# Kernel tuning notes

Hardware: AMD Instinct MI355X
Metric: run time of the kernel (lower is better)

Reference implementation:

```python
import jax, jax.numpy as jnp
import numpy as np

DIM, HEADS, DHEAD = 256, 8, 64
INNER = HEADS * DHEAD
EPS = 1e-5


def _ln(x, g, b):
    m = x.mean(-1, keepdims=True)
    v = ((x - m) ** 2).mean(-1, keepdims=True)
    return (x - m) / jnp.sqrt(v + EPS) * g + b


def setup_inputs() -> dict:
    key = jax.random.key(0)
    ks = jax.random.split(key, 24)
    b, n, Q, K = 1, 6, 900, 1408
    d = DIM
    s = lambda fan_in: 1.0 / np.sqrt(fan_in)
    inp = {
        "k_g": jax.random.normal(ks[0], (b, n, K, d), jnp.float32),
        "q_g": jax.random.normal(ks[1], (b, n, Q, d), jnp.float32),
        "k_a": jax.random.normal(ks[2], (b, n, K, d), jnp.float32),
        "q_a": jax.random.normal(ks[3], (b, Q, d), jnp.float32),
        "v": jax.random.normal(ks[4], (b, n, K, d), jnp.float32),
        "mask": jax.random.randint(ks[5], (b, n, K), 0, 2).astype(bool),
        # projections (stored as (in, out))
        "W_qg": jax.random.uniform(ks[6], (d, INNER), jnp.float32, -s(d), s(d)),
        "b_qg": jnp.zeros((INNER,), jnp.float32),
        "W_kg": jax.random.uniform(ks[7], (d, INNER), jnp.float32, -s(d), s(d)),
        "b_kg": jnp.zeros((INNER,), jnp.float32),
        "W_qa": jax.random.uniform(ks[8], (d, INNER), jnp.float32, -s(d), s(d)),
        "b_qa": jnp.zeros((INNER,), jnp.float32),
        "W_ka": jax.random.uniform(ks[9], (d, INNER), jnp.float32, -s(d), s(d)),
        "b_ka": jnp.zeros((INNER,), jnp.float32),
        "W_v": jax.random.uniform(ks[10], (d, INNER), jnp.float32, -s(d), s(d)),
        "b_v": jnp.zeros((INNER,), jnp.float32),
        "W_o": jax.random.uniform(ks[11], (INNER, d), jnp.float32, -s(INNER), s(INNER)),
        "b_o": jnp.zeros((d,), jnp.float32),
        "ln1_g": jnp.ones((d,), jnp.float32),
        "ln1_b": jnp.zeros((d,), jnp.float32),
        "W_m1": jax.random.uniform(ks[12], (d, 2 * d), jnp.float32, -s(d), s(d)),
        "b_m1": jnp.zeros((2 * d,), jnp.float32),
        "W_m2": jax.random.uniform(ks[13], (2 * d, d), jnp.float32, -s(2 * d), s(2 * d)),
        "b_m2": jnp.zeros((d,), jnp.float32),
        "ln2_g": jnp.ones((d,), jnp.float32),
        "ln2_b": jnp.zeros((d,), jnp.float32),
        "scale_g": jnp.full((HEADS,), DHEAD ** -0.5, jnp.float32),
        "scale_a": jnp.full((HEADS,), DHEAD ** -0.5, jnp.float32),
    }
    return inp


def reference(k_g, q_g, k_a, q_a, v, mask,
              W_qg, b_qg, W_kg, b_kg, W_qa, b_qa, W_ka, b_ka, W_v, b_v,
              W_o, b_o, ln1_g, ln1_b, W_m1, b_m1, W_m2, b_m2, ln2_g, ln2_b,
              scale_g, scale_a):
    b, n, Q, _ = q_g.shape
    K = k_g.shape[2]
    h, dh = HEADS, DHEAD
    skip = q_a

    def split(x):  # (..., h*dh) -> (b, h, ..., dh)
        return jnp.moveaxis(x.reshape(x.shape[:-1] + (h, dh)), -2, 1)

    kg = split(k_g @ W_kg + b_kg)          # (b, h, n, K, dh)
    qg = split(q_g @ W_qg + b_qg)          # (b, h, n, Q, dh)
    ka = split(k_a @ W_ka + b_ka)          # (b, h, n, K, dh)
    qa = split(q_a @ W_qa + b_qa)          # (b, h, Q, dh)
    vv = split(v @ W_v + b_v)              # (b, h, n, K, dh)

    dot_g = jnp.einsum('bhnqd,bhnkd->bhnqk', qg, kg)
    dot_a = jnp.einsum('bhqd,bhnkd->bhnqk', qa, ka)
    sg = scale_g[None, :, None, None, None]
    sa = scale_a[None, :, None, None, None]
    dot = sg * dot_g + sa * dot_a
    dot = jnp.where(mask[:, None, :, None, :], -jnp.inf, dot)

    # softmax jointly over (n, K)
    dot = dot.transpose(0, 1, 3, 2, 4).reshape(b, h, Q, n * K)
    att = jax.nn.softmax(dot, axis=-1)
    vflat = vv.reshape(b, h, n * K, dh)
    a = jnp.einsum('bhqk,bhkd->bhqd', att, vflat)
    a = a.transpose(0, 2, 1, 3).reshape(b, Q, h * dh)

    z = a @ W_o + b_o + skip
    z = _ln(z, ln1_g, ln1_b)
    z = z + (jax.nn.gelu(z @ W_m1 + b_m1, approximate=False) @ W_m2 + b_m2)
    z = _ln(z, ln2_g, ln2_b)
    return z
```

## Files before the change

kernel.cpp:

```cpp
#include <hip/hip_runtime.h>
#include <stdint.h>

typedef unsigned short u16;
typedef _Float16 half8 __attribute__((ext_vector_type(8)));
typedef float f32x4 __attribute__((ext_vector_type(4)));

__device__ __forceinline__ u16 f2h(float f) {
    _Float16 h = (_Float16)f; u16 u; __builtin_memcpy(&u, &h, 2); return u;
}
__device__ __forceinline__ float h2f(u16 u) {
    _Float16 h; __builtin_memcpy(&h, &u, 2); return (float)h;
}

template<int CTRL>
__device__ __forceinline__ float dppf(float x) {
    return __builtin_bit_cast(float,
        __builtin_amdgcn_update_dpp(0, __builtin_bit_cast(int, x), CTRL, 0xF, 0xF, false));
}
__device__ __forceinline__ float sum16(float x) {
    x += dppf<0xB1>(x);
    x += dppf<0x4E>(x);
    x += dppf<0x124>(x);
    x += dppf<0x128>(x);
    return x;
}

__global__ __launch_bounds__(256) void prep_kernel(
    const float* __restrict__ W_qg, const float* __restrict__ W_kg,
    const float* __restrict__ W_qa, const float* __restrict__ W_ka,
    const float* __restrict__ W_v,  const float* __restrict__ W_o,
    const float* __restrict__ W_m1, const float* __restrict__ W_m2,
    u16* __restrict__ T_qg, u16* __restrict__ T_kg, u16* __restrict__ T_qa,
    u16* __restrict__ T_ka, u16* __restrict__ T_v,  u16* __restrict__ T_o,
    u16* __restrict__ T_m1, u16* __restrict__ T_m2,
    const float* __restrict__ scale_g, const float* __restrict__ scale_a,
    const float* __restrict__ b_kg, const float* __restrict__ b_ka,
    float* __restrict__ bkg_s, float* __restrict__ bka_s,
    const int* __restrict__ mask, int* __restrict__ mflag)
{
    const int z = blockIdx.z;
    const int tid = threadIdx.x;
    if (z == 8) {
        if (blockIdx.y != 0) return;
        if (blockIdx.x == 0) {
            __shared__ int f;
            if (tid == 0) f = 0;
            __syncthreads();
            int local = 0;
            for (int i = tid; i < 2112; i += 256) { int vv = mask[i]; if (vv & ~1) local = 1; }
            if (local) atomicOr(&f, 1);
            __syncthreads();
            if (tid == 0) *mflag = f;
        } else if (blockIdx.x == 1) {
            for (int j = tid; j < 512; j += 256) {
                bkg_s[j] = b_kg[j] * scale_g[j >> 6];
                bka_s[j] = b_ka[j] * scale_a[j >> 6];
            }
        }
        return;
    }
    const int K = (z == 5 || z == 7) ? 512 : 256;
    const int N = (z == 5 || z == 7) ? 256 : 512;
    const int k0 = blockIdx.x * 64, n0 = blockIdx.y * 64;
    if (k0 >= K || n0 >= N) return;
    const float* W = z==0?W_qg: z==1?W_kg: z==2?W_qa: z==3?W_ka: z==4?W_v: z==5?W_o: z==6?W_m1: W_m2;
    u16* D        = z==0?T_qg: z==1?T_kg: z==2?T_qa: z==3?T_ka: z==4?T_v: z==5?T_o: z==6?T_m1: T_m2;
    const float* scp = z==1 ? scale_g : z==3 ? scale_a : nullptr;

    __shared__ u16 T[64][80];
    const int cr = tid >> 4, cc = (tid & 15) * 4;
    const float sc = scp ? scp[(n0 + cc) >> 6] : 1.0f;
    #pragma unroll
    for (int i = 0; i < 4; ++i) {
        const int r = cr + i * 16;
        const float4 vv = *(const float4*)(W + (size_t)(k0 + r) * N + n0 + cc);
        T[cc + 0][r] = f2h(vv.x * sc);
        T[cc + 1][r] = f2h(vv.y * sc);
        T[cc + 2][r] = f2h(vv.z * sc);
        T[cc + 3][r] = f2h(vv.w * sc);
    }
    __syncthreads();
    const int nr = tid >> 2, part = (tid & 3) * 16;
    u16* drow = D + (size_t)(n0 + nr) * K + k0 + part;
    *(half8*)(drow)     = *(const half8*)&T[nr][part];
    *(half8*)(drow + 8) = *(const half8*)&T[nr][part + 8];
}

__global__ __launch_bounds__(256, 4) void proj_all(
    const float* __restrict__ k_g, const float* __restrict__ k_a,
    const float* __restrict__ v,   const float* __restrict__ q_g,
    const float* __restrict__ q_a,
    const u16* __restrict__ T_kg, const u16* __restrict__ T_ka,
    const u16* __restrict__ T_v,  const u16* __restrict__ T_qg,
    const u16* __restrict__ T_qa,
    const float* __restrict__ bkg_s, const float* __restrict__ bka_s,
    const float* __restrict__ b_v,   const float* __restrict__ b_qg,
    const float* __restrict__ b_qa,
    u16* __restrict__ qcat, u16* __restrict__ kcat, u16* __restrict__ vt)
{
    __shared__ u16 Ws[256 * 36];

    int bx = blockIdx.x;
    int mode, M;
    const float* X; const u16* Wt; const float* bias; u16* out;
    if (bx < 132)      { mode = 2; M = 8448; X = k_g; Wt = T_kg; bias = bkg_s; out = kcat; }
    else if (bx < 264) { mode = 3; M = 8448; X = k_a; Wt = T_ka; bias = bka_s; out = kcat; bx -= 132; }
    else if (bx < 396) { mode = 4; M = 8448; X = v;   Wt = T_v;  bias = b_v;   out = vt;   bx -= 264; }
    else if (bx < 481) { mode = 0; M = 5400; X = q_g; Wt = T_qg; bias = b_qg;  out = qcat; bx -= 396; }
    else               { mode = 1; M = 900;  X = q_a; Wt = T_qa; bias = b_qa;  out = qcat; bx -= 481; }
    const int rows_per_n = (mode == 0) ? 900 : 1408;

    const int tid = threadIdx.x;
    const int w = tid >> 6, lane = tid & 63;
    const int l15 = lane & 15, quad = lane >> 4;
    const int m0 = bx * 64;
    const int nbase = blockIdx.y * 256;
    const int row = m0 + w * 16 + l15;

    const float* xrow = X + (size_t)(row < M ? row : 0) * 256 + quad * 8;
    const u16* wcol = Wt + ((size_t)(nbase + tid) << 8);

    f32x4 o[4][4];
    #pragma unroll
    for (int nt = 0; nt < 4; ++nt)
        #pragma unroll
        for (int t = 0; t < 4; ++t) { o[nt][t][0]=0.f; o[nt][t][1]=0.f; o[nt][t][2]=0.f; o[nt][t][3]=0.f; }

    for (int k0 = 0; k0 < 8; ++k0) {
        {
            const uint4 w0 = *(const uint4*)(wcol + k0 * 32 + 0);
            const uint4 w1 = *(const uint4*)(wcol + k0 * 32 + 8);
            const uint4 w2 = *(const uint4*)(wcol + k0 * 32 + 16);
            const uint4 w3 = *(const uint4*)(wcol + k0 * 32 + 24);
            *(uint4*)&Ws[tid * 36 + 0]  = w0;
            *(uint4*)&Ws[tid * 36 + 8]  = w1;
            *(uint4*)&Ws[tid * 36 + 16] = w2;
            *(uint4*)&Ws[tid * 36 + 24] = w3;
        }
        __syncthreads();

        const float4 a0 = *(const float4*)(xrow + k0 * 32);
        const float4 a1 = *(const float4*)(xrow + k0 * 32 + 4);
        half8 af;
        af[0]=(_Float16)a0.x; af[1]=(_Float16)a0.y; af[2]=(_Float16)a0.z; af[3]=(_Float16)a0.w;
        af[4]=(_Float16)a1.x; af[5]=(_Float16)a1.y; af[6]=(_Float16)a1.z; af[7]=(_Float16)a1.w;

        #pragma unroll
        for (int nt = 0; nt < 4; ++nt)
            #pragma unroll
            for (int t = 0; t < 4; ++t) {
                const half8 bf = *(const half8*)&Ws[(nt * 64 + t * 16 + l15) * 36 + quad * 8];
                o[nt][t] = __builtin_amdgcn_mfma_f32_16x16x32_f16(af, bf, o[nt][t], 0, 0, 0);
            }
        __syncthreads();
    }

    #pragma unroll
    for (int nt = 0; nt < 4; ++nt) {
        const int n0 = nbase + nt * 64;
        const int hh = n0 >> 6;
        float bj[4];
        #pragma unroll
        for (int t = 0; t < 4; ++t) bj[t] = bias[n0 + t * 16 + l15];

        if (mode == 4) {
            const int gr0 = m0 + w * 16 + quad * 4;
            if (gr0 < M) {
                const int nI = gr0 / rows_per_n;
                const int rr = gr0 - nI * rows_per_n;
                u16* vb = out + (size_t)(hh * 6 + nI) * 64 * 1408;
                #pragma unroll
                for (int t = 0; t < 4; ++t) {
                    const int d = t * 16 + l15;
                    ushort4 pk;
                    pk.x = f2h(o[nt][t][0] + bj[t]);
                    pk.y = f2h(o[nt][t][1] + bj[t]);
                    pk.z = f2h(o[nt][t][2] + bj[t]);
                    pk.w = f2h(o[nt][t][3] + bj[t]);
                    *(ushort4*)&vb[(size_t)d * 1408 + rr] = pk;
                }
            }
        } else if (mode == 1) {
            #pragma unroll
            for (int r = 0; r < 4; ++r) {
                const int gr = m0 + w * 16 + quad * 4 + r;
                if (gr < M) {
                    for (int nb = 0; nb < 6; ++nb) {
                        u16* qb = out + (((size_t)(hh * 6 + nb) * 900 + gr) << 7) + 64;
                        #pragma unroll
                        for (int t = 0; t < 4; ++t)
                            qb[t * 16 + l15] = f2h(o[nt][t][r] + bj[t]);
                    }
                }
            }
        } else {
            const size_t kdim = (mode == 0) ? 900 : 1408;
            const int doff = (mode == 3) ? 64 : 0;
            #pragma unroll
            for (int r = 0; r < 4; ++r) {
                const int gr = m0 + w * 16 + quad * 4 + r;
                if (gr < M) {
                    const int nI = gr / rows_per_n;
                    const int rr = gr - nI * rows_per_n;
                    u16* ob = out + (((size_t)(hh * 6 + nI) * kdim + rr) << 7) + doff;
                    #pragma unroll
                    for (int t = 0; t < 4; ++t)
                        ob[t * 16 + l15] = f2h(o[nt][t][r] + bj[t]);
                }
            }
        }
    }
}

__global__ __launch_bounds__(256, 3) void attn_kernel(
    const u16* __restrict__ qcat, const u16* __restrict__ kcat,
    const u16* __restrict__ vt, const void* __restrict__ maskp,
    const int* __restrict__ mflag,
    u16* __restrict__ Opart, float* __restrict__ lpart)
{
    __shared__ u16 Ks[64 * 132];
    __shared__ u16 Vs[64 * 68];
    __shared__ u16 Ps[4][16][72];
    __shared__ float Mb[64];

    const int flat = blockIdx.x;
    const int grp = flat >> 3;
    const int qt = grp % 15;
    const int rest = grp / 15;
    const int hn_i = (flat & 7) + 8 * (rest % 6);
    const int sp = rest / 6;
    const int h = hn_i / 6, n = hn_i - h * 6;

    const int q0 = qt * 64;
    const int tid = threadIdx.x;
    const int w = tid >> 6, lane = tid & 63;
    const int l15 = lane & 15, quad = lane >> 4;
    const bool m8 = (*mflag != 0);
    const size_t hn = (size_t)hn_i;

    const u16* kbase = kcat + ((hn * 1408) << 7);
    const u16* vbase = vt + hn * 64 * 1408;
    const unsigned char* mB = (const unsigned char*)maskp;
    const int* mI = (const int*)maskp;
    const int mko = n * 1408;

    const int krow_s = tid >> 4;
    const int kcol_s = (tid & 15) * 8;
    const int vrow_s = tid >> 3;
    const int vcol_s = (tid & 7) * 8;

    half8 qf[4];
    {
        const int gq = q0 + w * 16 + l15;
        if (gq < 900) {
            const u16* qrow = qcat + ((hn * 900 + gq) << 7) + quad * 8;
            #pragma unroll
            for (int k0 = 0; k0 < 4; ++k0)
                qf[k0] = *(const half8*)(qrow + k0 * 32);
        } else {
            #pragma unroll
            for (int k0 = 0; k0 < 4; ++k0)
                #pragma unroll
                for (int j = 0; j < 8; ++j) qf[k0][j] = (_Float16)0.0f;
        }
    }

    f32x4 o[4];
    float lr[4];
    #pragma unroll
    for (int t = 0; t < 4; ++t) { o[t][0]=0.f; o[t][1]=0.f; o[t][2]=0.f; o[t][3]=0.f; }
    #pragma unroll
    for (int r = 0; r < 4; ++r) lr[r] = 0.f;

    for (int cc = 0; cc < 11; ++cc) {
        const int k0c = (sp * 11 + cc) * 64;

        {
            const uint4 k0r = *(const uint4*)(kbase + ((size_t)(k0c +  0 + krow_s) << 7) + kcol_s);
            const uint4 k1r = *(const uint4*)(kbase + ((size_t)(k0c + 16 + krow_s) << 7) + kcol_s);
            const uint4 k2r = *(const uint4*)(kbase + ((size_t)(k0c + 32 + krow_s) << 7) + kcol_s);
            const uint4 k3r = *(const uint4*)(kbase + ((size_t)(k0c + 48 + krow_s) << 7) + kcol_s);
            const uint4 v0r = *(const uint4*)(vbase + (size_t)(vrow_s)      * 1408 + k0c + vcol_s);
            const uint4 v1r = *(const uint4*)(vbase + (size_t)(32 + vrow_s) * 1408 + k0c + vcol_s);
            *(uint4*)&Ks[( 0 + krow_s) * 132 + kcol_s] = k0r;
            *(uint4*)&Ks[(16 + krow_s) * 132 + kcol_s] = k1r;
            *(uint4*)&Ks[(32 + krow_s) * 132 + kcol_s] = k2r;
            *(uint4*)&Ks[(48 + krow_s) * 132 + kcol_s] = k3r;
            *(uint4*)&Vs[(vrow_s)      * 68 + vcol_s] = v0r;
            *(uint4*)&Vs[(32 + vrow_s) * 68 + vcol_s] = v1r;
            if (tid < 64) {
                const int ki = mko + k0c + tid;
                const int mv = m8 ? (int)mB[ki] : mI[ki];
                Mb[tid] = mv ? -1e30f : 0.0f;
            }
        }
        __syncthreads();

        f32x4 s[4];
        #pragma unroll
        for (int t = 0; t < 4; ++t) { s[t][0]=0.f; s[t][1]=0.f; s[t][2]=0.f; s[t][3]=0.f; }
        #pragma unroll
        for (int k0 = 0; k0 < 4; ++k0)
            #pragma unroll
            for (int t = 0; t < 4; ++t) {
                const half8 kf = *(const half8*)&Ks[(t * 16 + l15) * 132 + k0 * 32 + quad * 8];
                s[t] = __builtin_amdgcn_mfma_f32_16x16x32_f16(qf[k0], kf, s[t], 0, 0, 0);
            }

        #pragma unroll
        for (int t = 0; t < 4; ++t) {
            const float mbv = Mb[t * 16 + l15];
            s[t][0] += mbv; s[t][1] += mbv; s[t][2] += mbv; s[t][3] += mbv;
        }

        #pragma unroll
        for (int r = 0; r < 4; ++r) {
            const float p0 = __expf(s[0][r]);
            const float p1 = __expf(s[1][r]);
            const float p2 = __expf(s[2][r]);
            const float p3 = __expf(s[3][r]);
            lr[r] += sum16(p0 + p1 + p2 + p3);
            u16* pr = &Ps[w][quad * 4 + r][l15];
            pr[0]  = f2h(p0);
            pr[16] = f2h(p1);
            pr[32] = f2h(p2);
            pr[48] = f2h(p3);
        }

        const u16* prow = &Ps[w][l15][quad * 8];
        const half8 pa0 = *(const half8*)(prow);
        const half8 pa1 = *(const half8*)(prow + 32);
        #pragma unroll
        for (int t = 0; t < 4; ++t) {
            const half8 v0 = *(const half8*)&Vs[(t * 16 + l15) * 68 + quad * 8];
            const half8 v1 = *(const half8*)&Vs[(t * 16 + l15) * 68 + 32 + quad * 8];
            o[t] = __builtin_amdgcn_mfma_f32_16x16x32_f16(pa0, v0, o[t], 0, 0, 0);
            o[t] = __builtin_amdgcn_mfma_f32_16x16x32_f16(pa1, v1, o[t], 0, 0, 0);
        }
        __syncthreads();
    }

    const int p = sp * 48 + hn_i;
    #pragma unroll
    for (int r = 0; r < 4; ++r) {
        const int gq = q0 + w * 16 + quad * 4 + r;
        if (gq < 900) {
            u16* db = Opart + ((size_t)p * 900 + gq) * 64 + l15;
            db[0]  = f2h(o[0][r]);
            db[16] = f2h(o[1][r]);
            db[32] = f2h(o[2][r]);
            db[48] = f2h(o[3][r]);
            if (l15 == 0) lpart[p * 900 + gq] = lr[r];
        }
    }
}

__global__ __launch_bounds__(256) void combine_kernel(
    const u16* __restrict__ Opart, const float* __restrict__ lpart,
    u16* __restrict__ a16)
{
    const int g = blockIdx.x * 256 + threadIdx.x;
    const int h = g / 57600;
    const int r = g - h * 57600;
    const int q = r >> 6;
    const int d = r & 63;
    float l = 0.f, ov = 0.f;
    #pragma unroll
    for (int s = 0; s < 12; ++s) {
        const int p = (s >> 1) + h * 6 + ((s & 1) ? 48 : 0);
        l  += lpart[p * 900 + q];
        ov += h2f(Opart[((size_t)p * 900 + q) * 64 + d]);
    }
    a16[(size_t)q * 512 + h * 64 + d] = f2h(ov / fmaxf(l, 1e-30f));
}

__global__ __launch_bounds__(256) void epi_mega(
    const u16* __restrict__ a16, const u16* __restrict__ T_o,
    const u16* __restrict__ T_m1, const u16* __restrict__ T_m2,
    const float* __restrict__ b_o, const float* __restrict__ q_a,
    const float* __restrict__ ln1_g, const float* __restrict__ ln1_b,
    const float* __restrict__ b_m1, const float* __restrict__ b_m2,
    const float* __restrict__ ln2_g, const float* __restrict__ ln2_b,
    float* __restrict__ outf)
{
    __shared__ u16 Ws[512 * 36];
    __shared__ u16 Z1[16][264];
    __shared__ u16 H[16][520];
    __shared__ float Ssum[4][16];
    __shared__ float Ssq[4][16];

    const int tid = threadIdx.x;
    const int w = tid >> 6, lane = tid & 63;
    const int l15 = lane & 15, quad = lane >> 4;
    const int m0 = blockIdx.x * 16;

    {
        const int ar = m0 + l15;
        const u16* arow = a16 + (size_t)(ar < 900 ? ar : 899) * 512 + quad * 8;
        const u16* wcol = T_o + (size_t)tid * 512;

        f32x4 acc[4];
        #pragma unroll
        for (int t = 0; t < 4; ++t) { acc[t][0]=0.f; acc[t][1]=0.f; acc[t][2]=0.f; acc[t][3]=0.f; }

        for (int k0 = 0; k0 < 16; ++k0) {
            const uint4 w0 = *(const uint4*)(wcol + k0 * 32 + 0);
            const uint4 w1 = *(const uint4*)(wcol + k0 * 32 + 8);
            const uint4 w2 = *(const uint4*)(wcol + k0 * 32 + 16);
            const uint4 w3 = *(const uint4*)(wcol + k0 * 32 + 24);
            *(uint4*)&Ws[tid * 36 + 0]  = w0;
            *(uint4*)&Ws[tid * 36 + 8]  = w1;
            *(uint4*)&Ws[tid * 36 + 16] = w2;
            *(uint4*)&Ws[tid * 36 + 24] = w3;
            __syncthreads();
            const half8 af = *(const half8*)(arow + k0 * 32);
            #pragma unroll
            for (int t = 0; t < 4; ++t) {
                const half8 bf = *(const half8*)&Ws[(w * 64 + t * 16 + l15) * 36 + quad * 8];
                acc[t] = __builtin_amdgcn_mfma_f32_16x16x32_f16(af, bf, acc[t], 0, 0, 0);
            }
            __syncthreads();
        }

        float vals[4][4];
        #pragma unroll
        for (int r = 0; r < 4; ++r) {
            const int row = m0 + quad * 4 + r;
            const int rows = row < 900 ? row : 899;
            float s = 0.f, sq = 0.f;
            #pragma unroll
            for (int t = 0; t < 4; ++t) {
                const int col = w * 64 + t * 16 + l15;
                const float x = acc[t][r] + b_o[col] + q_a[(size_t)rows * 256 + col];
                vals[r][t] = x; s += x; sq += x * x;
            }
            s = sum16(s); sq = sum16(sq);
            if (l15 == 0) { Ssum[w][quad * 4 + r] = s; Ssq[w][quad * 4 + r] = sq; }
        }
        __syncthreads();

        #pragma unroll
        for (int r = 0; r < 4; ++r) {
            const int rl = quad * 4 + r;
            const float st = Ssum[0][rl] + Ssum[1][rl] + Ssum[2][rl] + Ssum[3][rl];
            const float qt = Ssq[0][rl] + Ssq[1][rl] + Ssq[2][rl] + Ssq[3][rl];
            const float mean = st * (1.0f / 256.0f);
            const float var  = qt * (1.0f / 256.0f) - mean * mean;
            const float inv  = rsqrtf(var + 1e-5f);
            #pragma unroll
            for (int t = 0; t < 4; ++t) {
                const int col = w * 64 + t * 16 + l15;
                const float z = (vals[r][t] - mean) * inv * ln1_g[col] + ln1_b[col];
                Z1[rl][col] = f2h(z);
            }
        }
        __syncthreads();
    }

    {
        const u16* wc0 = T_m1 + (size_t)tid * 256;
        const u16* wc1 = T_m1 + (size_t)(tid + 256) * 256;

        f32x4 acc[8];
        #pragma unroll
        for (int t = 0; t < 8; ++t) { acc[t][0]=0.f; acc[t][1]=0.f; acc[t][2]=0.f; acc[t][3]=0.f; }

        for (int k0 = 0; k0 < 8; ++k0) {
            const uint4 a0 = *(const uint4*)(wc0 + k0 * 32 + 0);
            const uint4 a1 = *(const uint4*)(wc0 + k0 * 32 + 8);
            const uint4 a2 = *(const uint4*)(wc0 + k0 * 32 + 16);
            const uint4 a3 = *(const uint4*)(wc0 + k0 * 32 + 24);
            const uint4 c0 = *(const uint4*)(wc1 + k0 * 32 + 0);
            const uint4 c1 = *(const uint4*)(wc1 + k0 * 32 + 8);
            const uint4 c2 = *(const uint4*)(wc1 + k0 * 32 + 16);
            const uint4 c3 = *(const uint4*)(wc1 + k0 * 32 + 24);
            *(uint4*)&Ws[tid * 36 + 0]  = a0;
            *(uint4*)&Ws[tid * 36 + 8]  = a1;
            *(uint4*)&Ws[tid * 36 + 16] = a2;
            *(uint4*)&Ws[tid * 36 + 24] = a3;
            *(uint4*)&Ws[(tid + 256) * 36 + 0]  = c0;
            *(uint4*)&Ws[(tid + 256) * 36 + 8]  = c1;
            *(uint4*)&Ws[(tid + 256) * 36 + 16] = c2;
            *(uint4*)&Ws[(tid + 256) * 36 + 24] = c3;
            __syncthreads();
            const half8 af = *(const half8*)&Z1[l15][k0 * 32 + quad * 8];
            #pragma unroll
            for (int t = 0; t < 8; ++t) {
                const half8 bf = *(const half8*)&Ws[(w * 128 + t * 16 + l15) * 36 + quad * 8];
                acc[t] = __builtin_amdgcn_mfma_f32_16x16x32_f16(af, bf, acc[t], 0, 0, 0);
            }
            __syncthreads();
        }

        #pragma unroll
        for (int r = 0; r < 4; ++r) {
            const int rl = quad * 4 + r;
            #pragma unroll
            for (int t = 0; t < 8; ++t) {
                const int col = w * 128 + t * 16 + l15;
                const float x = acc[t][r] + b_m1[col];
                H[rl][col] = f2h(0.5f * x * (1.0f + erff(x * 0.70710678118654752f)));
            }
        }
        __syncthreads();
    }

    {
        const u16* wcol = T_m2 + (size_t)tid * 512;

        f32x4 acc[4];
        #pragma unroll
        for (int t = 0; t < 4; ++t) { acc[t][0]=0.f; acc[t][1]=0.f; acc[t][2]=0.f; acc[t][3]=0.f; }

        for (int k0 = 0; k0 < 16; ++k0) {
            const uint4 w0 = *(const uint4*)(wcol + k0 * 32 + 0);
            const uint4 w1 = *(const uint4*)(wcol + k0 * 32 + 8);
            const uint4 w2 = *(const uint4*)(wcol + k0 * 32 + 16);
            const uint4 w3 = *(const uint4*)(wcol + k0 * 32 + 24);
            *(uint4*)&Ws[tid * 36 + 0]  = w0;
            *(uint4*)&Ws[tid * 36 + 8]  = w1;
            *(uint4*)&Ws[tid * 36 + 16] = w2;
            *(uint4*)&Ws[tid * 36 + 24] = w3;
            __syncthreads();
            const half8 af = *(const half8*)&H[l15][k0 * 32 + quad * 8];
            #pragma unroll
            for (int t = 0; t < 4; ++t) {
                const half8 bf = *(const half8*)&Ws[(w * 64 + t * 16 + l15) * 36 + quad * 8];
                acc[t] = __builtin_amdgcn_mfma_f32_16x16x32_f16(af, bf, acc[t], 0, 0, 0);
            }
            __syncthreads();
        }

        float vals[4][4];
        #pragma unroll
        for (int r = 0; r < 4; ++r) {
            const int rl = quad * 4 + r;
            float s = 0.f, sq = 0.f;
            #pragma unroll
            for (int t = 0; t < 4; ++t) {
                const int col = w * 64 + t * 16 + l15;
                const float x = acc[t][r] + b_m2[col] + h2f(Z1[rl][col]);
                vals[r][t] = x; s += x; sq += x * x;
            }
            s = sum16(s); sq = sum16(sq);
            if (l15 == 0) { Ssum[w][rl] = s; Ssq[w][rl] = sq; }
        }
        __syncthreads();

        #pragma unroll
        for (int r = 0; r < 4; ++r) {
            const int rl = quad * 4 + r;
            const float st = Ssum[0][rl] + Ssum[1][rl] + Ssum[2][rl] + Ssum[3][rl];
            const float qt = Ssq[0][rl] + Ssq[1][rl] + Ssq[2][rl] + Ssq[3][rl];
            const float mean = st * (1.0f / 256.0f);
            const float var  = qt * (1.0f / 256.0f) - mean * mean;
            const float inv  = rsqrtf(var + 1e-5f);
            const int row = m0 + rl;
            if (row < 900) {
                #pragma unroll
                for (int t = 0; t < 4; ++t) {
                    const int col = w * 64 + t * 16 + l15;
                    outf[(size_t)row * 256 + col] = (vals[r][t] - mean) * inv * ln2_g[col] + ln2_b[col];
                }
            }
        }
    }
}

extern "C" void kernel_launch(void* const* d_in, const int* in_sizes, int n_in,
                              void* d_out, int out_size, void* d_ws, size_t ws_size,
                              hipStream_t stream)
{
    const float* k_g  = (const float*)d_in[0];
    const float* q_g  = (const float*)d_in[1];
    const float* k_a  = (const float*)d_in[2];
    const float* q_a  = (const float*)d_in[3];
    const float* v    = (const float*)d_in[4];
    const void*  mask = d_in[5];
    const float* W_qg = (const float*)d_in[6];
    const float* b_qg = (const float*)d_in[7];
    const float* W_kg = (const float*)d_in[8];
    const float* b_kg = (const float*)d_in[9];
    const float* W_qa = (const float*)d_in[10];
    const float* b_qa = (const float*)d_in[11];
    const float* W_ka = (const float*)d_in[12];
    const float* b_ka = (const float*)d_in[13];
    const float* W_v  = (const float*)d_in[14];
    const float* b_v  = (const float*)d_in[15];
    const float* W_o  = (const float*)d_in[16];
    const float* b_o  = (const float*)d_in[17];
    const float* ln1_g = (const float*)d_in[18];
    const float* ln1_b = (const float*)d_in[19];
    const float* W_m1 = (const float*)d_in[20];
    const float* b_m1 = (const float*)d_in[21];
    const float* W_m2 = (const float*)d_in[22];
    const float* b_m2 = (const float*)d_in[23];
    const float* ln2_g = (const float*)d_in[24];
    const float* ln2_b = (const float*)d_in[25];
    const float* scale_g = (const float*)d_in[26];
    const float* scale_a = (const float*)d_in[27];

    char* ws = (char*)d_ws;
    size_t off = 0;
    auto alloc = [&](size_t bytes) -> void* {
        void* p = ws + off;
        off += (bytes + 255) & ~(size_t)255;
        return p;
    };
    u16*   qcat  = (u16*)  alloc((size_t)8 * 6 * 900  * 128 * 2);
    u16*   kcat  = (u16*)  alloc((size_t)8 * 6 * 1408 * 128 * 2);
    u16*   vt    = (u16*)  alloc((size_t)8 * 6 * 64 * 1408 * 2);
    u16*   a16   = (u16*)  alloc((size_t)900 * 512 * 2);
    u16*   Tw[8];
    for (int i = 0; i < 8; ++i) Tw[i] = (u16*)alloc((size_t)512 * 256 * 2);
    float* bkg_s = (float*)alloc((size_t)512 * 4);
    float* bka_s = (float*)alloc((size_t)512 * 4);
    int*   mflag = (int*)  alloc(256);
    u16*   Opart = (u16*)  alloc((size_t)96 * 900 * 64 * 2);
    float* lpart = (float*)alloc((size_t)96 * 900 * 4);

    prep_kernel<<<dim3(8, 8, 9), 256, 0, stream>>>(
        W_qg, W_kg, W_qa, W_ka, W_v, W_o, W_m1, W_m2,
        Tw[0], Tw[1], Tw[2], Tw[3], Tw[4], Tw[5], Tw[6], Tw[7],
        scale_g, scale_a, b_kg, b_ka, bkg_s, bka_s, (const int*)mask, mflag);

    proj_all<<<dim3(496, 2), 256, 0, stream>>>(
        k_g, k_a, v, q_g, q_a,
        Tw[1], Tw[3], Tw[4], Tw[0], Tw[2],
        bkg_s, bka_s, b_v, b_qg, b_qa,
        qcat, kcat, vt);

    attn_kernel<<<1440, 256, 0, stream>>>(qcat, kcat, vt, mask, mflag, Opart, lpart);
    combine_kernel<<<1800, 256, 0, stream>>>(Opart, lpart, a16);

    epi_mega<<<57, 256, 0, stream>>>(
        a16, Tw[5], Tw[6], Tw[7],
        b_o, q_a, ln1_g, ln1_b, b_m1, b_m2, ln2_g, ln2_b,
        (float*)d_out);
}
```

Baseline: 259.3 us.

## Prefetch next K/V tile into registers and compute row sums via MFMA

Measured after the change: 263.4 us. About the same (+1.6%).

```diff
diff --git a/kernel.cpp b/kernel.cpp
--- a/kernel.cpp
+++ b/kernel.cpp
@@ -212,15 +212,15 @@
     }
 }
 
-__global__ __launch_bounds__(256, 3) void attn_kernel(
+__global__ __launch_bounds__(256, 4) void attn_kernel(
     const u16* __restrict__ qcat, const u16* __restrict__ kcat,
     const u16* __restrict__ vt, const void* __restrict__ maskp,
     const int* __restrict__ mflag,
     u16* __restrict__ Opart, float* __restrict__ lpart)
 {
-    __shared__ u16 Ks[64 * 132];
-    __shared__ u16 Vs[64 * 68];
-    __shared__ u16 Ps[4][16][72];
+    __shared__ __align__(16) u16 Ks[64 * 136];
+    __shared__ __align__(16) u16 Vs[64 * 72];
+    __shared__ __align__(16) u16 Ps[4][1216];
     __shared__ float Mb[64];
 
     const int flat = blockIdx.x;
@@ -230,6 +230,7 @@
     const int hn_i = (flat & 7) + 8 * (rest % 6);
     const int sp = rest / 6;
     const int h = hn_i / 6, n = hn_i - h * 6;
+    (void)h;
 
     const int q0 = qt * 64;
     const int tid = threadIdx.x;
@@ -265,53 +266,74 @@
         }
     }
 
+    half8 onesb;
+    {
+        const _Float16 ov = (l15 == 0) ? (_Float16)1.0f : (_Float16)0.0f;
+        #pragma unroll
+        for (int j = 0; j < 8; ++j) onesb[j] = ov;
+    }
+
     f32x4 o[4];
-    float lr[4];
+    f32x4 l16;
     #pragma unroll
     for (int t = 0; t < 4; ++t) { o[t][0]=0.f; o[t][1]=0.f; o[t][2]=0.f; o[t][3]=0.f; }
-    #pragma unroll
-    for (int r = 0; r < 4; ++r) lr[r] = 0.f;
+    l16[0]=0.f; l16[1]=0.f; l16[2]=0.f; l16[3]=0.f;
+
+    uint4 kA, kB, kC, kD, vA, vB;
+    float mreg = 0.0f;
+    {
+        const int k0c = (sp * 11) * 64;
+        kA = *(const uint4*)(kbase + ((size_t)(k0c +  0 + krow_s) << 7) + kcol_s);
+        kB = *(const uint4*)(kbase + ((size_t)(k0c + 16 + krow_s) << 7) + kcol_s);
+        kC = *(const uint4*)(kbase + ((size_t)(k0c + 32 + krow_s) << 7) + kcol_s);
+        kD = *(const uint4*)(kbase + ((size_t)(k0c + 48 + krow_s) << 7) + kcol_s);
+        vA = *(const uint4*)(vbase + (size_t)(vrow_s)      * 1408 + k0c + vcol_s);
+        vB = *(const uint4*)(vbase + (size_t)(32 + vrow_s) * 1408 + k0c + vcol_s);
+        if (tid < 64) {
+            const int ki = mko + k0c + tid;
+            const int mv = m8 ? (int)mB[ki] : mI[ki];
+            mreg = mv ? -1e30f : 0.0f;
+        }
+    }
 
     for (int cc = 0; cc < 11; ++cc) {
-        const int k0c = (sp * 11 + cc) * 64;
-
-        {
-            const uint4 k0r = *(const uint4*)(kbase + ((size_t)(k0c +  0 + krow_s) << 7) + kcol_s);
-            const uint4 k1r = *(const uint4*)(kbase + ((size_t)(k0c + 16 + krow_s) << 7) + kcol_s);
-            const uint4 k2r = *(const uint4*)(kbase + ((size_t)(k0c + 32 + krow_s) << 7) + kcol_s);
-            const uint4 k3r = *(const uint4*)(kbase + ((size_t)(k0c + 48 + krow_s) << 7) + kcol_s);
-            const uint4 v0r = *(const uint4*)(vbase + (size_t)(vrow_s)      * 1408 + k0c + vcol_s);
-            const uint4 v1r = *(const uint4*)(vbase + (size_t)(32 + vrow_s) * 1408 + k0c + vcol_s);
-            *(uint4*)&Ks[( 0 + krow_s) * 132 + kcol_s] = k0r;
-            *(uint4*)&Ks[(16 + krow_s) * 132 + kcol_s] = k1r;
-            *(uint4*)&Ks[(32 + krow_s) * 132 + kcol_s] = k2r;
-            *(uint4*)&Ks[(48 + krow_s) * 132 + kcol_s] = k3r;
-            *(uint4*)&Vs[(vrow_s)      * 68 + vcol_s] = v0r;
-            *(uint4*)&Vs[(32 + vrow_s) * 68 + vcol_s] = v1r;
+        *(uint4*)&Ks[( 0 + krow_s) * 136 + kcol_s] = kA;
+        *(uint4*)&Ks[(16 + krow_s) * 136 + kcol_s] = kB;
+        *(uint4*)&Ks[(32 + krow_s) * 136 + kcol_s] = kC;
+        *(uint4*)&Ks[(48 + krow_s) * 136 + kcol_s] = kD;
+        *(uint4*)&Vs[(vrow_s)      * 72 + vcol_s] = vA;
+        *(uint4*)&Vs[(32 + vrow_s) * 72 + vcol_s] = vB;
+        if (tid < 64) Mb[tid] = mreg;
+        __syncthreads();
+
+        if (cc < 10) {
+            const int k0n = (sp * 11 + cc + 1) * 64;
+            kA = *(const uint4*)(kbase + ((size_t)(k0n +  0 + krow_s) << 7) + kcol_s);
+            kB = *(const uint4*)(kbase + ((size_t)(k0n + 16 + krow_s) << 7) + kcol_s);
+            kC = *(const uint4*)(kbase + ((size_t)(k0n + 32 + krow_s) << 7) + kcol_s);
+            kD = *(const uint4*)(kbase + ((size_t)(k0n + 48 + krow_s) << 7) + kcol_s);
+            vA = *(const uint4*)(vbase + (size_t)(vrow_s)      * 1408 + k0n + vcol_s);
+            vB = *(const uint4*)(vbase + (size_t)(32 + vrow_s) * 1408 + k0n + vcol_s);
             if (tid < 64) {
-                const int ki = mko + k0c + tid;
+                const int ki = mko + k0n + tid;
                 const int mv = m8 ? (int)mB[ki] : mI[ki];
-                Mb[tid] = mv ? -1e30f : 0.0f;
-            }
-        }
-        __syncthreads();
+                mreg = mv ? -1e30f : 0.0f;
+            }
+        }
 
         f32x4 s[4];
-        #pragma unroll
-        for (int t = 0; t < 4; ++t) { s[t][0]=0.f; s[t][1]=0.f; s[t][2]=0.f; s[t][3]=0.f; }
-        #pragma unroll
-        for (int k0 = 0; k0 < 4; ++k0)
-            #pragma unroll
-            for (int t = 0; t < 4; ++t) {
-                const half8 kf = *(const half8*)&Ks[(t * 16 + l15) * 132 + k0 * 32 + quad * 8];
-                s[t] = __builtin_amdgcn_mfma_f32_16x16x32_f16(qf[k0], kf, s[t], 0, 0, 0);
-            }
-
         #pragma unroll
         for (int t = 0; t < 4; ++t) {
             const float mbv = Mb[t * 16 + l15];
-            s[t][0] += mbv; s[t][1] += mbv; s[t][2] += mbv; s[t][3] += mbv;
-        }
+            s[t][0]=mbv; s[t][1]=mbv; s[t][2]=mbv; s[t][3]=mbv;
+        }
+        #pragma unroll
+        for (int k0 = 0; k0 < 4; ++k0)
+            #pragma unroll
+            for (int t = 0; t < 4; ++t) {
+                const half8 kf = *(const half8*)&Ks[(t * 16 + l15) * 136 + k0 * 32 + quad * 8];
+                s[t] = __builtin_amdgcn_mfma_f32_16x16x32_f16(qf[k0], kf, s[t], 0, 0, 0);
+            }
 
         #pragma unroll
         for (int r = 0; r < 4; ++r) {
@@ -319,21 +341,24 @@
             const float p1 = __expf(s[1][r]);
             const float p2 = __expf(s[2][r]);
             const float p3 = __expf(s[3][r]);
-            lr[r] += sum16(p0 + p1 + p2 + p3);
-            u16* pr = &Ps[w][quad * 4 + r][l15];
+            u16* pr = &Ps[w][(quad * 4 + r) * 72 + quad * 16 + l15];
             pr[0]  = f2h(p0);
             pr[16] = f2h(p1);
             pr[32] = f2h(p2);
             pr[48] = f2h(p3);
         }
 
-        const u16* prow = &Ps[w][l15][quad * 8];
+        const u16* prow = &Ps[w][l15 * 72 + (l15 >> 2) * 16 + quad * 8];
         const half8 pa0 = *(const half8*)(prow);
         const half8 pa1 = *(const half8*)(prow + 32);
+
+        l16 = __builtin_amdgcn_mfma_f32_16x16x32_f16(pa0, onesb, l16, 0, 0, 0);
+        l16 = __builtin_amdgcn_mfma_f32_16x16x32_f16(pa1, onesb, l16, 0, 0, 0);
+
         #pragma unroll
         for (int t = 0; t < 4; ++t) {
-            const half8 v0 = *(const half8*)&Vs[(t * 16 + l15) * 68 + quad * 8];
-            const half8 v1 = *(const half8*)&Vs[(t * 16 + l15) * 68 + 32 + quad * 8];
+            const half8 v0 = *(const half8*)&Vs[(t * 16 + l15) * 72 + quad * 8];
+            const half8 v1 = *(const half8*)&Vs[(t * 16 + l15) * 72 + 32 + quad * 8];
             o[t] = __builtin_amdgcn_mfma_f32_16x16x32_f16(pa0, v0, o[t], 0, 0, 0);
             o[t] = __builtin_amdgcn_mfma_f32_16x16x32_f16(pa1, v1, o[t], 0, 0, 0);
         }
@@ -350,7 +375,7 @@
             db[16] = f2h(o[1][r]);
             db[32] = f2h(o[2][r]);
             db[48] = f2h(o[3][r]);
-            if (l15 == 0) lpart[p * 900 + gq] = lr[r];
+            if (l15 == 0) lpart[p * 900 + gq] = l16[r];
         }
     }
 }
```
